# Kernel tuning notes

Measured on AMD Instinct MI355X. Metric: run time of the kernel, lower is better.

Reference implementation:

```python
import jax, jax.numpy as jnp
import numpy as np

HIDDEN = 2048
N_HEADS = 16
N_KV = 4
HEAD_DIM = 128
EPS = 1e-6
B, S = 2, 2048


def rms_norm(x, w, eps=EPS):
    xf = x.astype(jnp.float32)
    var = jnp.mean(xf * xf, axis=-1, keepdims=True)
    return (w * (xf * jax.lax.rsqrt(var + eps))).astype(x.dtype)


def rotate_half(x):
    half = x.shape[-1] // 2
    return jnp.concatenate([-x[..., half:], x[..., :half]], axis=-1)


def setup_inputs() -> dict:
    key = jax.random.key(0)
    ks = jax.random.split(key, 9)
    inv_freq = 1.0 / (10000.0 ** (np.arange(0, HEAD_DIM, 2) / HEAD_DIM))
    ang = np.arange(S)[:, None] * inv_freq[None, :]
    ang = np.concatenate([ang, ang], axis=-1)  # [S, HEAD_DIM]
    return {
        "hidden_states": jax.random.normal(ks[0], (B, S, HIDDEN), jnp.float32),
        "cos": jnp.asarray(np.cos(ang), jnp.float32),
        "sin": jnp.asarray(np.sin(ang), jnp.float32),
        "Wq": jax.random.normal(ks[1], (HIDDEN, N_HEADS * HEAD_DIM), jnp.float32) * 0.02,
        "Wk": jax.random.normal(ks[2], (HIDDEN, N_KV * HEAD_DIM), jnp.float32) * 0.02,
        "Wv": jax.random.normal(ks[3], (HIDDEN, N_KV * HEAD_DIM), jnp.float32) * 0.02,
        "Wo": jax.random.normal(ks[4], (N_HEADS * HEAD_DIM, HIDDEN), jnp.float32) * 0.02,
        "q_norm_w": jnp.ones((HEAD_DIM,), jnp.float32),
        "k_norm_w": jnp.ones((HEAD_DIM,), jnp.float32),
    }


def reference(hidden_states, cos, sin, Wq, Wk, Wv, Wo, q_norm_w, k_norm_w):
    b, s, _ = hidden_states.shape
    n_rep = N_HEADS // N_KV
    scaling = HEAD_DIM ** -0.5

    q = (hidden_states @ Wq).reshape(b, s, N_HEADS, HEAD_DIM)
    k = (hidden_states @ Wk).reshape(b, s, N_KV, HEAD_DIM)
    v = (hidden_states @ Wv).reshape(b, s, N_KV, HEAD_DIM)

    q = rms_norm(q, q_norm_w)
    k = rms_norm(k, k_norm_w)

    q = q.transpose(0, 2, 1, 3)  # [b, h, s, d]
    k = k.transpose(0, 2, 1, 3)  # [b, kv, s, d]
    v = v.transpose(0, 2, 1, 3)

    c = cos[None, None]  # [1,1,s,d]
    si = sin[None, None]
    q = q * c + rotate_half(q) * si
    k = k * c + rotate_half(k) * si

    # repeat kv heads to match query heads
    k = jnp.repeat(k, n_rep, axis=1)
    v = jnp.repeat(v, n_rep, axis=1)

    scores = jnp.einsum("bhqd,bhkd->bhqk", q, k) * scaling
    causal = jnp.triu(jnp.full((s, s), -jnp.inf, jnp.float32), k=1)
    scores = scores + causal
    attn = jax.nn.softmax(scores.astype(jnp.float32), axis=-1).astype(q.dtype)

    out = jnp.einsum("bhqk,bhkd->bhqd", attn, v)
    out = out.transpose(0, 2, 1, 3).reshape(b, s, N_HEADS * HEAD_DIM)
    return out @ Wo
```

## Files before the change

### kernel.cpp

```cpp
#include <hip/hip_runtime.h>

typedef float floatx4 __attribute__((ext_vector_type(4)));
typedef short short8 __attribute__((ext_vector_type(8)));

#define HIDDEN 2048
#define NH 16
#define NKV 4
#define HD 128
#define NB 2
#define SEQ 2048
#define MT (NB * SEQ)
#define NQKV 3072

__device__ __forceinline__ unsigned short f2bf(float x) {
  union { float f; unsigned u; } v; v.f = x;
  unsigned r = v.u + 0x7FFFu + ((v.u >> 16) & 1u);
  return (unsigned short)(r >> 16);
}

__global__ void cast_bf16_kernel(const float* __restrict__ in,
                                 unsigned short* __restrict__ out, int n4) {
  int i = blockIdx.x * 256 + threadIdx.x;
  if (i >= n4) return;
  float4 v = ((const float4*)in)[i];
  ushort4 o;
  o.x = f2bf(v.x); o.y = f2bf(v.y); o.z = f2bf(v.z); o.w = f2bf(v.w);
  ((ushort4*)out)[i] = o;
}

__global__ void wtrans_kernel(const float* __restrict__ Wq,
                              const float* __restrict__ Wk,
                              const float* __restrict__ Wv,
                              const float* __restrict__ Wo,
                              unsigned short* __restrict__ wqkvt,
                              unsigned short* __restrict__ wot) {
  __shared__ float tile[32][33];
  int z = blockIdx.z;
  int nt = blockIdx.x * 32;
  int k0 = blockIdx.y * 32;
  const float* src;
  unsigned short* dst;
  int Nd, scol0, drow0;
  if (z == 0) {
    src = Wq; Nd = 2048; scol0 = nt; drow0 = nt; dst = wqkvt;
  } else if (z == 1) {
    src = Wo; Nd = 2048; scol0 = nt; drow0 = nt; dst = wot;
  } else {
    if (nt >= 1024) return;
    Nd = 512; dst = wqkvt; drow0 = 2048 + nt;
    if (nt < 512) { src = Wk; scol0 = nt; }
    else          { src = Wv; scol0 = nt - 512; }
  }
  int tx = threadIdx.x, ty = threadIdx.y;
  for (int i = 0; i < 32; i += 8)
    tile[ty + i][tx] = src[(size_t)(k0 + ty + i) * Nd + scol0 + tx];
  __syncthreads();
  for (int i = 0; i < 32; i += 8)
    dst[(size_t)(drow0 + ty + i) * HIDDEN + k0 + tx] = f2bf(tile[tx][ty + i]);
}

__global__ __launch_bounds__(256, 3)
void gemm_bf16_kernel(const unsigned short* __restrict__ A,
                      const unsigned short* __restrict__ Bt,
                      float* __restrict__ C, int M, int N, int K) {
  __shared__ unsigned short As[128 * 32];
  __shared__ unsigned short Bs[128 * 32];
  const int tid = threadIdx.x;
  const int wave = tid >> 6, lane = tid & 63;
  const int quad = lane >> 4, l16 = lane & 15;
  const int m0 = blockIdx.x * 128, n0 = blockIdx.y * 128;
  const int wm = (wave >> 1) * 64, wn = (wave & 1) * 64;
  const int srow = lane >> 2;
  const int scol = (lane & 3) * 8;

  floatx4 acc[4][4] = {};

  for (int kt = 0; kt < K; kt += 32) {
    __syncthreads();
#pragma unroll
    for (int t = 0; t < 2; ++t) {
      int q = wave * 2 + t;
      int row = q * 16 + srow;
      __builtin_amdgcn_global_load_lds(
          (const __attribute__((address_space(1))) unsigned int*)&A[(size_t)(m0 + row) * K + kt + scol],
          (__attribute__((address_space(3))) unsigned int*)&As[q * 16 * 32],
          16, 0, 0);
      __builtin_amdgcn_global_load_lds(
          (const __attribute__((address_space(1))) unsigned int*)&Bt[(size_t)(n0 + row) * K + kt + scol],
          (__attribute__((address_space(3))) unsigned int*)&Bs[q * 16 * 32],
          16, 0, 0);
    }
    __syncthreads();
    short8 af[4], bf[4];
#pragma unroll
    for (int i = 0; i < 4; i++)
      af[i] = *(const short8*)&As[(wm + i * 16 + l16) * 32 + quad * 8];
#pragma unroll
    for (int j = 0; j < 4; j++)
      bf[j] = *(const short8*)&Bs[(wn + j * 16 + l16) * 32 + quad * 8];
#pragma unroll
    for (int i = 0; i < 4; i++)
#pragma unroll
      for (int j = 0; j < 4; j++)
        acc[i][j] = __builtin_amdgcn_mfma_f32_16x16x32_bf16(af[i], bf[j], acc[i][j], 0, 0, 0);
  }
#pragma unroll
  for (int i = 0; i < 4; i++) {
    int row = m0 + wm + i * 16 + quad * 4;
#pragma unroll
    for (int j = 0; j < 4; j++) {
      int col = n0 + wn + j * 16 + l16;
#pragma unroll
      for (int r = 0; r < 4; r++)
        C[(size_t)(row + r) * N + col] = acc[i][j][r];
    }
  }
}

__global__ __launch_bounds__(256, 3)
void gemm_qkv_kernel(const unsigned short* __restrict__ A,
                     const unsigned short* __restrict__ Bt,
                     const float* __restrict__ qw,
                     const float* __restrict__ kw,
                     const float* __restrict__ cosb,
                     const float* __restrict__ sinb,
                     unsigned short* __restrict__ Qb,
                     unsigned short* __restrict__ Kbb,
                     unsigned short* __restrict__ Vt) {
  __shared__ __align__(16) unsigned short As[128 * 32];
  __shared__ __align__(16) unsigned short Bs[128 * 32];
  __shared__ __align__(16) float pscr[4 * 64 * 20];
  __shared__ float pssq[2][128];
  const int tid = threadIdx.x;
  const int wave = tid >> 6, lane = tid & 63;
  const int quad = lane >> 4, l16 = lane & 15;
  const int m0 = blockIdx.x * 128, n0 = blockIdx.y * 128;
  const int wm = (wave >> 1) * 64, wn = (wave & 1) * 64;
  const int srow = lane >> 2;
  const int scol = (lane & 3) * 8;

  floatx4 acc[4][4] = {};

  for (int kt = 0; kt < HIDDEN; kt += 32) {
    __syncthreads();
#pragma unroll
    for (int t = 0; t < 2; ++t) {
      int q = wave * 2 + t;
      int row = q * 16 + srow;
      __builtin_amdgcn_global_load_lds(
          (const __attribute__((address_space(1))) unsigned int*)&A[(size_t)(m0 + row) * HIDDEN + kt + scol],
          (__attribute__((address_space(3))) unsigned int*)&As[q * 16 * 32],
          16, 0, 0);
      __builtin_amdgcn_global_load_lds(
          (const __attribute__((address_space(1))) unsigned int*)&Bt[(size_t)(n0 + row) * HIDDEN + kt + scol],
          (__attribute__((address_space(3))) unsigned int*)&Bs[q * 16 * 32],
          16, 0, 0);
    }
    __syncthreads();
    short8 af[4], bf[4];
#pragma unroll
    for (int i = 0; i < 4; i++)
      af[i] = *(const short8*)&As[(wm + i * 16 + l16) * 32 + quad * 8];
#pragma unroll
    for (int j = 0; j < 4; j++)
      bf[j] = *(const short8*)&Bs[(wn + j * 16 + l16) * 32 + quad * 8];
#pragma unroll
    for (int i = 0; i < 4; i++)
#pragma unroll
      for (int j = 0; j < 4; j++)
        acc[i][j] = __builtin_amdgcn_mfma_f32_16x16x32_bf16(af[i], bf[j], acc[i][j], 0, 0, 0);
  }

  const int head = n0 >> 7;
  if (head >= NH + NKV) {
    const int kv = head - (NH + NKV);
#pragma unroll
    for (int i = 0; i < 4; ++i) {
      int m = m0 + wm + i * 16 + quad * 4;
      int b = m >> 11, sbase = m & (SEQ - 1);
#pragma unroll
      for (int j = 0; j < 4; ++j) {
        int d = wn + j * 16 + l16;
        ushort4 pk;
        pk.x = f2bf(acc[i][j][0]); pk.y = f2bf(acc[i][j][1]);
        pk.z = f2bf(acc[i][j][2]); pk.w = f2bf(acc[i][j][3]);
        *(ushort4*)&Vt[((size_t)(b * NKV + kv) * HD + d) * SEQ + sbase] = pk;
      }
    }
    return;
  }

  const float* w = (head < NH) ? qw : kw;
  float wown[4], wpar[4];
#pragma unroll
  for (int j = 0; j < 4; ++j) {
    wown[j] = w[wn + j * 16 + l16];
    wpar[j] = w[(wn ^ 64) + j * 16 + l16];
  }
#pragma unroll
  for (int i = 0; i < 4; ++i) {
    float sq[4];
#pragma unroll
    for (int r = 0; r < 4; ++r) {
      float s2 = acc[i][0][r] * acc[i][0][r] + acc[i][1][r] * acc[i][1][r] +
                 acc[i][2][r] * acc[i][2][r] + acc[i][3][r] * acc[i][3][r];
#pragma unroll
      for (int off = 1; off < 16; off <<= 1) s2 += __shfl_xor(s2, off, 64);
      sq[r] = s2;
    }
    if (l16 == 0)
      *(float4*)&pssq[wn >> 6][wm + i * 16 + quad * 4] = make_float4(sq[0], sq[1], sq[2], sq[3]);
#pragma unroll
    for (int j = 0; j < 4; ++j)
      *(float4*)&pscr[(wave * 64 + j * 16 + l16) * 20 + quad * 4] = *(float4*)&acc[i][j];
    __syncthreads();
    float4 oss = *(const float4*)&pssq[(wn >> 6) ^ 1][wm + i * 16 + quad * 4];
    float rr[4];
    rr[0] = rsqrtf((sq[0] + oss.x) * (1.0f / 128.0f) + 1e-6f);
    rr[1] = rsqrtf((sq[1] + oss.y) * (1.0f / 128.0f) + 1e-6f);
    rr[2] = rsqrtf((sq[2] + oss.z) * (1.0f / 128.0f) + 1e-6f);
    rr[3] = rsqrtf((sq[3] + oss.w) * (1.0f / 128.0f) + 1e-6f);
    int mbase = m0 + wm + i * 16 + quad * 4;
    int b = mbase >> 11, sbase = mbase & (SEQ - 1);
#pragma unroll
    for (int j = 0; j < 4; ++j) {
      float4 par = *(const float4*)&pscr[((wave ^ 1) * 64 + j * 16 + l16) * 20 + quad * 4];
      float pr[4] = {par.x, par.y, par.z, par.w};
      int d = wn + j * 16 + l16;
      unsigned short* dst = (head < NH)
          ? Qb + ((size_t)(b * NH + head) * SEQ + sbase) * HD + d
          : Kbb + ((size_t)(b * NKV + (head - NH)) * SEQ + sbase) * HD + d;
#pragma unroll
      for (int r = 0; r < 4; ++r) {
        int s = sbase + r;
        float c = cosb[s * HD + d], sn = sinb[s * HD + d];
        float xo = acc[i][j][r] * rr[r] * wown[j];
        float xp = pr[r] * rr[r] * wpar[j];
        float out = (wn == 0) ? (xo * c - xp * sn) : (xo * c + xp * sn);
        dst[(size_t)r * HD] = f2bf(out);
      }
    }
    __syncthreads();
  }
}

#define LQ 136

__global__ __launch_bounds__(256, 3)
void attn_kernel(const unsigned short* __restrict__ Q,
                 const unsigned short* __restrict__ Kb,
                 const unsigned short* __restrict__ Vt,
                 unsigned short* __restrict__ O) {
  __shared__ unsigned short KVs[128 * LQ];
  __shared__ unsigned short Ps[64 * LQ];
  const int tid = threadIdx.x;
  const int wave = tid >> 6, lane = tid & 63;
  const int quad = lane >> 4, l16 = lane & 15;
  const int qt = (SEQ / 64 - 1) - (blockIdx.x >> 5);
  const int bh = blockIdx.x & 31;
  const int b = bh >> 4, h = bh & 15, kvh = h >> 2;
  const int q0 = qt * 64;
  const int nkt = (qt >> 1) + 1;

  const unsigned short* Qg = Q + (size_t)((b * NH + h) * SEQ + q0) * HD;
  short8 qf[4];
#pragma unroll
  for (int ks = 0; ks < 4; ++ks)
    qf[ks] = *(const short8*)&Qg[(size_t)(wave * 16 + l16) * HD + ks * 32 + quad * 8];

  floatx4 oacc[8] = {};
  float mrow[4] = {-1e30f, -1e30f, -1e30f, -1e30f};
  float lrow[4] = {0.f, 0.f, 0.f, 0.f};
  const float scale = 0.08838834764831845f;
  const unsigned short* Kg0 = Kb + (size_t)((b * NKV + kvh) * SEQ) * HD;
  const unsigned short* Vg0 = Vt + (size_t)((b * NKV + kvh) * HD) * SEQ;

  for (int kt = 0; kt < nkt; ++kt) {
    __syncthreads();
    for (int c = tid; c < 2048; c += 256) {
      int r = c >> 4, c8 = c & 15;
      *(uint4*)&KVs[r * LQ + c8 * 8] = *(const uint4*)&Kg0[(size_t)(kt * 128 + r) * HD + c8 * 8];
    }
    __syncthreads();
    floatx4 sc[8] = {};
#pragma unroll
    for (int ks = 0; ks < 4; ++ks) {
#pragma unroll
      for (int j = 0; j < 8; ++j) {
        short8 bf = *(const short8*)&KVs[(j * 16 + l16) * LQ + ks * 32 + quad * 8];
        sc[j] = __builtin_amdgcn_mfma_f32_16x16x32_bf16(qf[ks], bf, sc[j], 0, 0, 0);
      }
    }
#pragma unroll
    for (int j = 0; j < 8; ++j)
#pragma unroll
      for (int r = 0; r < 4; ++r) sc[j][r] *= scale;
    if (kt == nkt - 1) {
      int rowg = q0 + wave * 16 + quad * 4;
#pragma unroll
      for (int j = 0; j < 8; ++j) {
        int col = kt * 128 + j * 16 + l16;
#pragma unroll
        for (int r = 0; r < 4; ++r)
          if (col > rowg + r) sc[j][r] = -1e30f;
      }
    }
    float alpha[4];
#pragma unroll
    for (int r = 0; r < 4; ++r) {
      float mx = sc[0][r];
#pragma unroll
      for (int j = 1; j < 8; ++j) mx = fmaxf(mx, sc[j][r]);
#pragma unroll
      for (int off = 1; off < 16; off <<= 1) mx = fmaxf(mx, __shfl_xor(mx, off, 64));
      float mn = fmaxf(mrow[r], mx);
      alpha[r] = __expf(mrow[r] - mn);
      mrow[r] = mn;
      float rs = 0.f;
#pragma unroll
      for (int j = 0; j < 8; ++j) {
        float p = __expf(sc[j][r] - mn);
        sc[j][r] = p;
        rs += p;
      }
#pragma unroll
      for (int off = 1; off < 16; off <<= 1) rs += __shfl_xor(rs, off, 64);
      lrow[r] = lrow[r] * alpha[r] + rs;
    }
#pragma unroll
    for (int t = 0; t < 8; ++t)
#pragma unroll
      for (int r = 0; r < 4; ++r) oacc[t][r] *= alpha[r];
#pragma unroll
    for (int j = 0; j < 8; ++j)
#pragma unroll
      for (int r = 0; r < 4; ++r)
        Ps[(wave * 16 + quad * 4 + r) * LQ + j * 16 + l16] = f2bf(sc[j][r]);
    __syncthreads();
    for (int c = tid; c < 2048; c += 256) {
      int d = c >> 4, c8 = c & 15;
      *(uint4*)&KVs[d * LQ + c8 * 8] = *(const uint4*)&Vg0[(size_t)d * SEQ + kt * 128 + c8 * 8];
    }
    __syncthreads();
#pragma unroll
    for (int ks = 0; ks < 4; ++ks) {
      short8 af = *(const short8*)&Ps[(wave * 16 + l16) * LQ + ks * 32 + quad * 8];
#pragma unroll
      for (int t = 0; t < 8; ++t) {
        short8 bf = *(const short8*)&KVs[(t * 16 + l16) * LQ + ks * 32 + quad * 8];
        oacc[t] = __builtin_amdgcn_mfma_f32_16x16x32_bf16(af, bf, oacc[t], 0, 0, 0);
      }
    }
  }
  float inv[4];
#pragma unroll
  for (int r = 0; r < 4; ++r) inv[r] = 1.0f / lrow[r];
#pragma unroll
  for (int t = 0; t < 8; ++t) {
    int col = h * HD + t * 16 + l16;
#pragma unroll
    for (int r = 0; r < 4; ++r) {
      int row = q0 + wave * 16 + quad * 4 + r;
      O[(size_t)(b * SEQ + row) * (NH * HD) + col] = f2bf(oacc[t][r] * inv[r]);
    }
  }
}

extern "C" void kernel_launch(void* const* d_in, const int* in_sizes, int n_in,
                              void* d_out, int out_size, void* d_ws, size_t ws_size,
                              hipStream_t stream) {
  const float* hidden = (const float*)d_in[0];
  const float* cosb   = (const float*)d_in[1];
  const float* sinb   = (const float*)d_in[2];
  const float* Wq     = (const float*)d_in[3];
  const float* Wk     = (const float*)d_in[4];
  const float* Wv     = (const float*)d_in[5];
  const float* Wo     = (const float*)d_in[6];
  const float* qw     = (const float*)d_in[7];
  const float* kw     = (const float*)d_in[8];
  (void)in_sizes; (void)n_in; (void)out_size; (void)ws_size;

  char* ws = (char*)d_ws;
  size_t off = 0;
  auto alloc = [&](size_t n) { char* p = ws + off; off += (n + 255) & ~(size_t)255; return p; };

  unsigned short* hb    = (unsigned short*)alloc((size_t)MT * HIDDEN * 2);
  unsigned short* wqkvt = (unsigned short*)alloc((size_t)NQKV * HIDDEN * 2);
  unsigned short* wot   = (unsigned short*)alloc((size_t)2048 * 2048 * 2);
  unsigned short* Qb  = (unsigned short*)alloc((size_t)MT * 2048 * 2);
  unsigned short* Kbb = (unsigned short*)alloc((size_t)MT * 512 * 2);
  unsigned short* Vtb = (unsigned short*)alloc((size_t)MT * 512 * 2);
  unsigned short* Ob  = (unsigned short*)alloc((size_t)MT * 2048 * 2);

  cast_bf16_kernel<<<(MT * HIDDEN / 4) / 256, 256, 0, stream>>>(hidden, hb, MT * HIDDEN / 4);
  dim3 tb(32, 8);
  wtrans_kernel<<<dim3(64, 64, 3), tb, 0, stream>>>(Wq, Wk, Wv, Wo, wqkvt, wot);

  gemm_qkv_kernel<<<dim3(MT / 128, NQKV / 128), 256, 0, stream>>>(
      hb, wqkvt, qw, kw, cosb, sinb, Qb, Kbb, Vtb);

  attn_kernel<<<(SEQ / 64) * 32, 256, 0, stream>>>(Qb, Kbb, Vtb, Ob);

  gemm_bf16_kernel<<<dim3(MT / 128, 16), 256, 0, stream>>>(Ob, wot, (float*)d_out, MT, 2048, 2048);
}
```

Baseline: 336.9 us.

## Rewrite attention kernel with async LDS loads, swizzling, and paired query tiles

Rewrites the attention kernel. K/V tiles are now loaded with direct global-to-LDS loads into a double-buffered, XOR-swizzled layout, and the next K tile is prefetched while softmax runs. Scores are computed transposed (S^T = K·Q), so the bf16-packed probabilities stay in registers as the MFMA A operand instead of going through shared memory. Each block handles a long and a short causal query tile (qt and 31-qt) to balance work, and the grid drops to 512 blocks. The online softmax only rescales the accumulator when the row maximum grows past a threshold. The risks are the intricate swizzle and fragment-index bookkeeping, lower occupancy (launch bound 2), and an inline-asm conversion tied to the ISA.

```diff
diff --git a/kernel.cpp b/kernel.cpp
--- a/kernel.cpp
+++ b/kernel.cpp
@@ -16,6 +16,12 @@
   union { float f; unsigned u; } v; v.f = x;
   unsigned r = v.u + 0x7FFFu + ((v.u >> 16) & 1u);
   return (unsigned short)(r >> 16);
+}
+
+__device__ __forceinline__ unsigned int cvt_pk_bf16(float lo, float hi) {
+  unsigned int r;
+  asm("v_cvt_pk_bf16_f32 %0, %1, %2" : "=v"(r) : "v"(lo), "v"(hi));
+  return r;
 }
 
 __global__ void cast_bf16_kernel(const float* __restrict__ in,
@@ -244,124 +250,156 @@
   }
 }
 
-#define LQ 136
-
-__global__ __launch_bounds__(256, 3)
+
+__device__ __forceinline__ void stage_rows(const unsigned short* gbase, int rowstride,
+                                           unsigned short* lds, int wave, int quad,
+                                           int s_cx, int s_hb) {
+#pragma unroll
+  for (int i = 0; i < 8; ++i) {
+    const int row = i * 16 + wave * 4 + quad;
+    const int sck = s_cx ^ (((2 * i + s_hb) & 3) << 2);
+    __builtin_amdgcn_global_load_lds(
+        (const __attribute__((address_space(1))) unsigned int*)(gbase + (size_t)row * rowstride + sck * 8),
+        (__attribute__((address_space(3))) unsigned int*)(lds + (i * 4 + wave) * 512),
+        16, 0, 0);
+  }
+}
+
+__global__ __launch_bounds__(256, 2)
 void attn_kernel(const unsigned short* __restrict__ Q,
                  const unsigned short* __restrict__ Kb,
                  const unsigned short* __restrict__ Vt,
                  unsigned short* __restrict__ O) {
-  __shared__ unsigned short KVs[128 * LQ];
-  __shared__ unsigned short Ps[64 * LQ];
+  __shared__ __align__(16) unsigned short KVs[2][128 * 128];
   const int tid = threadIdx.x;
   const int wave = tid >> 6, lane = tid & 63;
   const int quad = lane >> 4, l16 = lane & 15;
-  const int qt = (SEQ / 64 - 1) - (blockIdx.x >> 5);
+  const int l3 = l16 & 3, s3 = l16 >> 3, s2 = (l16 >> 2) & 1;
   const int bh = blockIdx.x & 31;
+  const int pr = blockIdx.x >> 5;
   const int b = bh >> 4, h = bh & 15, kvh = h >> 2;
-  const int q0 = qt * 64;
-  const int nkt = (qt >> 1) + 1;
-
-  const unsigned short* Qg = Q + (size_t)((b * NH + h) * SEQ + q0) * HD;
-  short8 qf[4];
-#pragma unroll
-  for (int ks = 0; ks < 4; ++ks)
-    qf[ks] = *(const short8*)&Qg[(size_t)(wave * 16 + l16) * HD + ks * 32 + quad * 8];
-
-  floatx4 oacc[8] = {};
-  float mrow[4] = {-1e30f, -1e30f, -1e30f, -1e30f};
-  float lrow[4] = {0.f, 0.f, 0.f, 0.f};
-  const float scale = 0.08838834764831845f;
+
+  const int s_cx = (lane & 15) ^ quad;
+  const int s_hb = wave >> 1;
+  const int krbase = 16 * s3 + 8 * s2 + l3;
+  const int f_k = l3 | ((2 * s3 + s2) << 2);
+  const int kvqb = 16 * (quad >> 1) + 8 * (quad & 1);
+  const int qsw = (lane & 48) | (quad << 2);
+  const float CS = 0.08838834764831845f;
+
   const unsigned short* Kg0 = Kb + (size_t)((b * NKV + kvh) * SEQ) * HD;
   const unsigned short* Vg0 = Vt + (size_t)((b * NKV + kvh) * HD) * SEQ;
 
-  for (int kt = 0; kt < nkt; ++kt) {
-    __syncthreads();
-    for (int c = tid; c < 2048; c += 256) {
-      int r = c >> 4, c8 = c & 15;
-      *(uint4*)&KVs[r * LQ + c8 * 8] = *(const uint4*)&Kg0[(size_t)(kt * 128 + r) * HD + c8 * 8];
-    }
-    __syncthreads();
-    floatx4 sc[8] = {};
-#pragma unroll
-    for (int ks = 0; ks < 4; ++ks) {
+  int p = 0;
+#pragma unroll 1
+  for (int seg = 0; seg < 2; ++seg) {
+    const int qt = seg ? pr : (31 - pr);
+    const int q0 = qt * 64;
+    const int nkt = (qt >> 1) + 1;
+    const int qglob = q0 + wave * 16 + l16;
+
+    const unsigned short* Qg = Q + (size_t)((b * NH + h) * SEQ + q0) * HD;
+    short8 qf[4];
+#pragma unroll
+    for (int ks = 0; ks < 4; ++ks)
+      qf[ks] = *(const short8*)&Qg[(size_t)(wave * 16 + l16) * HD + ks * 32 + quad * 8];
+
+    floatx4 oacc[8] = {};
+    float mrow = -1e30f, lrow = 0.f;
+
+    stage_rows(Kg0, 128, KVs[p], wave, quad, s_cx, s_hb);
+    __syncthreads();
+
+    for (int kt = 0; kt < nkt; ++kt) {
+      const unsigned short* KVp = KVs[p];
+      floatx4 sc[8] = {};
+#pragma unroll
+      for (int ks = 0; ks < 4; ++ks) {
+        const int cko = ((ks * 4 + quad) ^ f_k) * 8;
+#pragma unroll
+        for (int j = 0; j < 8; ++j) {
+          const short8 kf = *(const short8*)&KVp[(krbase + 32 * (j >> 1) + 4 * (j & 1)) * 128 + cko];
+          sc[j] = __builtin_amdgcn_mfma_f32_16x16x32_bf16(kf, qf[ks], sc[j], 0, 0, 0);
+        }
+      }
+      __syncthreads();
+      stage_rows(Vg0 + kt * 128, SEQ, KVs[p], wave, quad, s_cx, s_hb);
+      if (kt + 1 < nkt)
+        stage_rows(Kg0 + (size_t)(kt + 1) * 128 * HD, 128, KVs[p ^ 1], wave, quad, s_cx, s_hb);
+
+      if (kt == nkt - 1) {
+#pragma unroll
+        for (int j = 0; j < 8; ++j) {
+          const int kvj = kt * 128 + 32 * (j >> 1) + 4 * (j & 1) + kvqb;
+#pragma unroll
+          for (int r = 0; r < 4; ++r)
+            if (kvj + r > qglob) sc[j][r] = -1e30f;
+        }
+      }
+      float mx = -1e30f;
+#pragma unroll
+      for (int j = 0; j < 8; ++j)
+        mx = fmaxf(mx, fmaxf(fmaxf(sc[j][0], sc[j][1]), fmaxf(sc[j][2], sc[j][3])));
+      mx = fmaxf(mx, __shfl_xor(mx, 16, 64));
+      mx = fmaxf(mx, __shfl_xor(mx, 32, 64));
+      if (!__all(mx <= mrow + 62.0f)) {
+        const float mnew = fmaxf(mrow, mx);
+        const float al = __expf((mrow - mnew) * CS);
+        mrow = mnew;
+        lrow *= al;
+#pragma unroll
+        for (int r = 0; r < 4; ++r) {
+          const float ar = __shfl(al, qsw + r, 64);
+#pragma unroll
+          for (int t = 0; t < 8; ++t) oacc[t][r] *= ar;
+        }
+      }
+      const float mc = mrow * CS;
+      float rs = 0.f;
+#pragma unroll
+      for (int j = 0; j < 8; ++j)
+#pragma unroll
+        for (int r = 0; r < 4; ++r) {
+          const float pe = __expf(sc[j][r] * CS - mc);
+          sc[j][r] = pe;
+          rs += pe;
+        }
+      rs += __shfl_xor(rs, 16, 64);
+      rs += __shfl_xor(rs, 32, 64);
+      lrow += rs;
+
+      unsigned int pk[8][2];
 #pragma unroll
       for (int j = 0; j < 8; ++j) {
-        short8 bf = *(const short8*)&KVs[(j * 16 + l16) * LQ + ks * 32 + quad * 8];
-        sc[j] = __builtin_amdgcn_mfma_f32_16x16x32_bf16(qf[ks], bf, sc[j], 0, 0, 0);
-      }
-    }
-#pragma unroll
-    for (int j = 0; j < 8; ++j)
-#pragma unroll
-      for (int r = 0; r < 4; ++r) sc[j][r] *= scale;
-    if (kt == nkt - 1) {
-      int rowg = q0 + wave * 16 + quad * 4;
-#pragma unroll
-      for (int j = 0; j < 8; ++j) {
-        int col = kt * 128 + j * 16 + l16;
-#pragma unroll
-        for (int r = 0; r < 4; ++r)
-          if (col > rowg + r) sc[j][r] = -1e30f;
-      }
-    }
-    float alpha[4];
-#pragma unroll
-    for (int r = 0; r < 4; ++r) {
-      float mx = sc[0][r];
-#pragma unroll
-      for (int j = 1; j < 8; ++j) mx = fmaxf(mx, sc[j][r]);
-#pragma unroll
-      for (int off = 1; off < 16; off <<= 1) mx = fmaxf(mx, __shfl_xor(mx, off, 64));
-      float mn = fmaxf(mrow[r], mx);
-      alpha[r] = __expf(mrow[r] - mn);
-      mrow[r] = mn;
-      float rs = 0.f;
-#pragma unroll
-      for (int j = 0; j < 8; ++j) {
-        float p = __expf(sc[j][r] - mn);
-        sc[j][r] = p;
-        rs += p;
-      }
-#pragma unroll
-      for (int off = 1; off < 16; off <<= 1) rs += __shfl_xor(rs, off, 64);
-      lrow[r] = lrow[r] * alpha[r] + rs;
-    }
-#pragma unroll
-    for (int t = 0; t < 8; ++t)
-#pragma unroll
-      for (int r = 0; r < 4; ++r) oacc[t][r] *= alpha[r];
-#pragma unroll
-    for (int j = 0; j < 8; ++j)
-#pragma unroll
-      for (int r = 0; r < 4; ++r)
-        Ps[(wave * 16 + quad * 4 + r) * LQ + j * 16 + l16] = f2bf(sc[j][r]);
-    __syncthreads();
-    for (int c = tid; c < 2048; c += 256) {
-      int d = c >> 4, c8 = c & 15;
-      *(uint4*)&KVs[d * LQ + c8 * 8] = *(const uint4*)&Vg0[(size_t)d * SEQ + kt * 128 + c8 * 8];
-    }
-    __syncthreads();
-#pragma unroll
-    for (int ks = 0; ks < 4; ++ks) {
-      short8 af = *(const short8*)&Ps[(wave * 16 + l16) * LQ + ks * 32 + quad * 8];
-#pragma unroll
-      for (int t = 0; t < 8; ++t) {
-        short8 bf = *(const short8*)&KVs[(t * 16 + l16) * LQ + ks * 32 + quad * 8];
-        oacc[t] = __builtin_amdgcn_mfma_f32_16x16x32_bf16(af, bf, oacc[t], 0, 0, 0);
-      }
-    }
-  }
-  float inv[4];
-#pragma unroll
-  for (int r = 0; r < 4; ++r) inv[r] = 1.0f / lrow[r];
-#pragma unroll
-  for (int t = 0; t < 8; ++t) {
-    int col = h * HD + t * 16 + l16;
-#pragma unroll
-    for (int r = 0; r < 4; ++r) {
-      int row = q0 + wave * 16 + quad * 4 + r;
-      O[(size_t)(b * SEQ + row) * (NH * HD) + col] = f2bf(oacc[t][r] * inv[r]);
+        pk[j][0] = cvt_pk_bf16(sc[j][0], sc[j][1]);
+        pk[j][1] = cvt_pk_bf16(sc[j][2], sc[j][3]);
+      }
+      __syncthreads();
+#pragma unroll
+      for (int ks = 0; ks < 4; ++ks) {
+        union { unsigned int u[4]; short8 s; } au;
+        au.u[0] = pk[2 * ks][0];     au.u[1] = pk[2 * ks][1];
+        au.u[2] = pk[2 * ks + 1][0]; au.u[3] = pk[2 * ks + 1][1];
+#pragma unroll
+        for (int t = 0; t < 8; ++t) {
+          const int fv = l3 | (((2 * t + s3) & 3) << 2);
+          const short8 vf = *(const short8*)&KVp[(t * 16 + l16) * 128 + (((ks * 4 + quad) ^ fv) * 8)];
+          oacc[t] = __builtin_amdgcn_mfma_f32_16x16x32_bf16(au.s, vf, oacc[t], 0, 0, 0);
+        }
+      }
+      p ^= 1;
+    }
+    float li[4];
+#pragma unroll
+    for (int r = 0; r < 4; ++r) li[r] = 1.0f / __shfl(lrow, qsw + r, 64);
+#pragma unroll
+    for (int t = 0; t < 8; ++t) {
+      const int col = h * HD + t * 16 + l16;
+#pragma unroll
+      for (int r = 0; r < 4; ++r) {
+        const int row = q0 + wave * 16 + quad * 4 + r;
+        O[(size_t)(b * SEQ + row) * (NH * HD) + col] = f2bf(oacc[t][r] * li[r]);
+      }
     }
   }
 }
@@ -399,7 +437,7 @@
   gemm_qkv_kernel<<<dim3(MT / 128, NQKV / 128), 256, 0, stream>>>(
       hb, wqkvt, qw, kw, cosb, sinb, Qb, Kbb, Vtb);
 
-  attn_kernel<<<(SEQ / 64) * 32, 256, 0, stream>>>(Qb, Kbb, Vtb, Ob);
+  attn_kernel<<<512, 256, 0, stream>>>(Qb, Kbb, Vtb, Ob);
 
   gemm_bf16_kernel<<<dim3(MT / 128, 16), 256, 0, stream>>>(Ob, wot, (float*)d_out, MT, 2048, 2048);
 }
```

Result: faster. 294.5 us (-12.6%).
